# Performance work log

Hardware: AMD Instinct MI355X
Metric: run time of the kernel (lower is better)

## Reference

```python
import jax, jax.numpy as jnp
import numpy as np
import math

N_HEADS = 16  # matches init_kwargs n_heads


def setup_inputs() -> dict:
    key = jax.random.key(0)
    k1, k2, k3 = jax.random.split(key, 3)
    B, S, D = 8, 1024, 1024
    x = jax.random.normal(k1, (B, S, D), dtype=jnp.float32)
    Wc = jax.random.normal(k2, (D, 3 * D), dtype=jnp.float32) * 0.02
    bc = jnp.zeros((3 * D,), dtype=jnp.float32)
    Wo = jax.random.normal(k3, (D, D), dtype=jnp.float32) * 0.02
    bo = jnp.zeros((D,), dtype=jnp.float32)
    return {"x": x, "Wc": Wc, "bc": bc, "Wo": Wo, "bo": bo}


def reference(x, Wc, bc, Wo, bo):
    B, S, D = x.shape
    H = N_HEADS
    hd = D // H
    qkv = x @ Wc + bc                         # [B,S,3D]
    q, k, v = jnp.split(qkv, 3, axis=2)
    q = q.reshape(B, S, H, hd)
    k = k.reshape(B, S, H, hd)
    v = v.reshape(B, S, H, hd)
    # NOTE: source scales by sqrt(d_size), not sqrt(head_dim)
    scores = jnp.einsum("bqhd,bkhd->bhqk", q, k) / math.sqrt(D)
    # source mask: triu(ones) kept, zeros (k < q) filled with float32 min
    # i.e. attend only to positions k >= q (anti-causal, faithful to source)
    keep = jnp.triu(jnp.ones((S, S), dtype=bool))  # [S,S]
    neg = jnp.finfo(jnp.float32).min
    scores = jnp.where(keep[None, None, :, :], scores, neg)
    attn = jax.nn.softmax(scores, axis=-1)    # [B,H,S,S]; dropout p=0 -> identity
    out = jnp.einsum("bhqk,bkhd->bqhd", attn, v)
    concat = out.reshape(B, S, D)
    return concat @ Wo + bo                   # final dropout p=0 -> identity
```

## Files before the change

kernel.cpp:

```cpp
#include <hip/hip_runtime.h>
#include <stdint.h>

typedef __attribute__((ext_vector_type(8))) short  bf16x8;
typedef __attribute__((ext_vector_type(4))) short  short4v;
typedef __attribute__((ext_vector_type(4))) float  f32x4;
typedef __attribute__((ext_vector_type(4))) float  float4v;

#define VMW(N) asm volatile("s_waitcnt vmcnt(" #N ")" ::: "memory")
#define BAR()  asm volatile("s_barrier" ::: "memory")

__device__ __forceinline__ short f2bf(float f) {
  union { float f; uint32_t u; } c; c.f = f;
  uint32_t u = c.u;
  uint32_t r = (u + 0x7FFFu + ((u >> 16) & 1u)) >> 16;
  return (short)(uint16_t)r;
}

__device__ __forceinline__ short f2bf_hw(float f) {
  return __builtin_bit_cast(short, (__bf16)f);
}

__device__ __forceinline__ void gload_lds16(const void* g, void* l) {
  __builtin_amdgcn_global_load_lds(
      (const __attribute__((address_space(1))) void*)g,
      (__attribute__((address_space(3))) void*)l, 16, 0, 0);
}

__global__ __launch_bounds__(256) void k_f32_to_bf16(
    const float* __restrict__ in, short* __restrict__ out, int n4) {
  int i = blockIdx.x * 256 + threadIdx.x;
  if (i >= n4) return;
  float4v v = *(const float4v*)(in + (size_t)i * 4);
  short4v o;
  o.x = f2bf(v.x); o.y = f2bf(v.y); o.z = f2bf(v.z); o.w = f2bf(v.w);
  *(short4v*)(out + (size_t)i * 4) = o;
}

__global__ __launch_bounds__(256) void k_transpose_bf16(
    const float* __restrict__ in, short* __restrict__ out, int R, int C) {
  __shared__ short tile[64][65];
  int bc = blockIdx.x * 64, br = blockIdx.y * 64;
  int tc = threadIdx.x & 63, tr = threadIdx.x >> 6;
#pragma unroll
  for (int i = 0; i < 64; i += 4)
    tile[tc][tr + i] = f2bf(in[(size_t)(br + tr + i) * C + bc + tc]);
  __syncthreads();
#pragma unroll
  for (int i = 0; i < 64; i += 4)
    out[(size_t)(bc + tr + i) * R + br + tc] = tile[tr + i][tc];
}

template <bool F32OUT>
__global__ __launch_bounds__(256) void k_gemm2(
    const short* __restrict__ A, const short* __restrict__ BT,
    const float* __restrict__ bias, void* __restrict__ Cout,
    int M, int N, int K, int nbn) {
  __shared__ short SM[2][2][2][128][32];
  const int tid = threadIdx.x;
  const int w = tid >> 6, l = tid & 63;
  const int fr = l & 15, fg = l >> 4;
  const int wm = w >> 1, wn = w & 1;

  const int q8 = gridDim.x >> 3;
  const int wg = (blockIdx.x & 7) * q8 + (blockIdx.x >> 3);
  const int bm = wg / nbn, bn = wg % nbn;
  const size_t brow = (size_t)bm << 7;
  const int bcol = bn << 7;

  const int NT = K >> 6;

  const int srow = l >> 2;
  const int soct = (l & 3) ^ ((l >> 3) & 3);
  const short* aG = A + (brow + srow) * (size_t)K + soct * 8;
  const short* bG = BT + ((size_t)(bcol + srow)) * K + soct * 8;
  const int slot8 = ((fg ^ ((fr >> 1) & 3)) << 3);

  f32x4 acc[4][4] = {};

#pragma unroll
  for (int s = 0; s < 6; ++s) {
    const int t = s >> 2, tau = s & 3, buf = t & 1, mat = tau & 1, kh = tau >> 1;
    const int kbase = t * 64 + kh * 32;
    const short* g0 = (mat ? bG : aG) + kbase;
#pragma unroll
    for (int j = 0; j < 2; ++j) {
      const int r0 = (w * 2 + j) * 16;
      gload_lds16(g0 + (size_t)r0 * K, (char*)&SM[buf][mat][kh][r0][0]);
    }
  }
  VMW(8);
  BAR();

  int sidx = 6;
  for (int t = 0; t < NT; ++t) {
    const int buf = t & 1;
#pragma unroll
    for (int p = 0; p < 2; ++p) {
      const int kh = p;
#pragma unroll
      for (int s = 0; s < 2; ++s) {
        if (sidx < NT * 4) {
          const int ts = sidx >> 2, tau = sidx & 3;
          const int sb = ts & 1, mat = tau & 1, skh = tau >> 1;
          const int kbase = ts * 64 + skh * 32;
          const short* g0 = (mat ? bG : aG) + kbase;
#pragma unroll
          for (int j = 0; j < 2; ++j) {
            const int r0 = (w * 2 + j) * 16;
            gload_lds16(g0 + (size_t)r0 * K, (char*)&SM[sb][mat][skh][r0][0]);
          }
          ++sidx;
        }
      }
      bf16x8 af[4], bf[4];
#pragma unroll
      for (int m = 0; m < 4; ++m)
        af[m] = *(const bf16x8*)&SM[buf][0][kh][wm * 64 + m * 16 + fr][slot8];
#pragma unroll
      for (int n = 0; n < 4; ++n)
        bf[n] = *(const bf16x8*)&SM[buf][1][kh][wn * 64 + n * 16 + fr][slot8];
      BAR();
      __builtin_amdgcn_s_setprio(1);
#pragma unroll
      for (int m = 0; m < 4; ++m)
#pragma unroll
        for (int n = 0; n < 4; ++n)
          acc[m][n] = __builtin_amdgcn_mfma_f32_16x16x32_bf16(
              af[m], bf[n], acc[m][n], 0, 0, 0);
      __builtin_amdgcn_s_setprio(0);
      if (!(t == NT - 1 && p == 1)) {
        if (t == NT - 1 && p == 0) { VMW(0); }
        else if (t == NT - 2 && p == 1) { VMW(4); }
        else { VMW(8); }
        BAR();
      }
    }
  }

#pragma unroll
  for (int n = 0; n < 4; ++n) {
    const int col = bcol + wn * 64 + n * 16 + fr;
    const float bv = bias[col];
#pragma unroll
    for (int i = 0; i < 4; ++i) {
      const size_t row = brow + (size_t)(wm * 64 + i * 16 + fg * 4);
#pragma unroll
      for (int r = 0; r < 4; ++r) {
        const float v = acc[i][n][r] + bv;
        if (F32OUT)
          ((float*)Cout)[(row + r) * (size_t)N + col] = v;
        else
          ((short*)Cout)[(row + r) * (size_t)N + col] = f2bf(v);
      }
    }
  }
}

__global__ __launch_bounds__(256) void k_attn(
    const short* __restrict__ qkv, short* __restrict__ outc, int Bn, int S) {
  __shared__ short Ks[128][64];
  __shared__ short Vt[64][136];

  const int tid = threadIdx.x;
  const int w = tid >> 6, l = tid & 63;
  const int fr = l & 15, fg = l >> 4;

  const int tq = blockIdx.x >> 7;
  const int bh = blockIdx.x & 127;
  const int h = bh & 15, b = bh >> 4;
  const int q0 = tq << 6;

  const size_t rowbase = (size_t)b * S;
  const int qcol = q0 + w * 16 + fr;

  bf16x8 qf[2];
  {
    const short* qp = qkv + (rowbase + qcol) * 3072 + h * 64 + fg * 8;
    qf[0] = *(const bf16x8*)qp;
    qf[1] = *(const bf16x8*)(qp + 32);
    const float C2 = 0.04508422f;
#pragma unroll
    for (int j = 0; j < 8; ++j) {
      union { float f; uint32_t u; } ca, cb;
      ca.u = ((uint32_t)(uint16_t)qf[0][j]) << 16;
      cb.u = ((uint32_t)(uint16_t)qf[1][j]) << 16;
      qf[0][j] = f2bf_hw(ca.f * C2);
      qf[1][j] = f2bf_hw(cb.f * C2);
    }
  }

  f32x4 o[4] = {};
  float lacc = 0.0f;

  const short* Kbase = qkv + rowbase * 3072 + 1024 + h * 64;
  const short* Vbase = qkv + rowbase * 3072 + 2048 + h * 64;

  const int c0 = tq >> 1;
  for (int c = c0; c < 8; ++c) {
    const int k0 = c << 7;
    {
      int r8 = l >> 3, slot = l & 7;
#pragma unroll
      for (int j = 0; j < 4; ++j) {
        int ch = w * 4 + j;
        int row = ch * 8 + r8;
        int d = (slot ^ (row & 7)) << 3;
        gload_lds16(Kbase + (size_t)(k0 + row) * 3072 + d,
                    (char*)&Ks[0][0] + ch * 1024);
      }
    }
    {
      int db = (tid >> 4) << 2;
#pragma unroll
      for (int kh = 0; kh < 2; ++kh) {
        int kb = ((tid & 15) << 2) + (kh << 6);
        const short* vp = Vbase + (size_t)(k0 + kb) * 3072 + db;
        short4v r0 = *(const short4v*)(vp);
        short4v r1 = *(const short4v*)(vp + 3072);
        short4v r2 = *(const short4v*)(vp + 2 * 3072);
        short4v r3 = *(const short4v*)(vp + 3 * 3072);
        short4v t0 = {r0.x, r1.x, r2.x, r3.x};
        short4v t1 = {r0.y, r1.y, r2.y, r3.y};
        short4v t2 = {r0.z, r1.z, r2.z, r3.z};
        short4v t3 = {r0.w, r1.w, r2.w, r3.w};
        *(short4v*)&Vt[db + 0][kb] = t0;
        *(short4v*)&Vt[db + 1][kb] = t1;
        *(short4v*)&Vt[db + 2][kb] = t2;
        *(short4v*)&Vt[db + 3][kb] = t3;
      }
    }
    __syncthreads();

    f32x4 st[8];
#pragma unroll
    for (int kb = 0; kb < 8; ++kb) {
      f32x4 z = {0.f, 0.f, 0.f, 0.f};
      int row = kb * 16 + fr;
      int sw = row & 7;
      bf16x8 kf0 = *(const bf16x8*)&Ks[row][(fg ^ sw) << 3];
      bf16x8 kf1 = *(const bf16x8*)&Ks[row][((4 + fg) ^ sw) << 3];
      z = __builtin_amdgcn_mfma_f32_16x16x32_bf16(kf0, qf[0], z, 0, 0, 0);
      z = __builtin_amdgcn_mfma_f32_16x16x32_bf16(kf1, qf[1], z, 0, 0, 0);
      st[kb] = z;
    }

    const bool masked = (c == c0);
#pragma unroll
    for (int kb = 0; kb < 8; ++kb)
#pragma unroll
      for (int r = 0; r < 4; ++r) {
        float e = exp2f(st[kb][r]);
        if (masked) {
          int kg = k0 + kb * 16 + fg * 4 + r;
          e = (kg < qcol) ? 0.0f : e;
        }
        st[kb][r] = e;
        lacc += e;
      }

#pragma unroll
    for (int kb2 = 0; kb2 < 4; ++kb2) {
      bf16x8 pa = {f2bf_hw(st[2 * kb2][0]),     f2bf_hw(st[2 * kb2][1]),
                   f2bf_hw(st[2 * kb2][2]),     f2bf_hw(st[2 * kb2][3]),
                   f2bf_hw(st[2 * kb2 + 1][0]), f2bf_hw(st[2 * kb2 + 1][1]),
                   f2bf_hw(st[2 * kb2 + 1][2]), f2bf_hw(st[2 * kb2 + 1][3])};
#pragma unroll
      for (int f = 0; f < 4; ++f) {
        short4v v0 = *(const short4v*)&Vt[f * 16 + fr][kb2 * 32 + fg * 4];
        short4v v1 = *(const short4v*)&Vt[f * 16 + fr][kb2 * 32 + 16 + fg * 4];
        bf16x8 vb = {v0.x, v0.y, v0.z, v0.w, v1.x, v1.y, v1.z, v1.w};
        o[f] = __builtin_amdgcn_mfma_f32_16x16x32_bf16(pa, vb, o[f], 0, 0, 0);
      }
    }
    __syncthreads();
  }

  lacc += __shfl_xor(lacc, 16, 64);
  lacc += __shfl_xor(lacc, 32, 64);
#pragma unroll
  for (int r = 0; r < 4; ++r) {
    float denom = __shfl(lacc, fg * 4 + r, 64);
    float inv = 1.0f / denom;
    size_t orow = rowbase + (size_t)(q0 + w * 16 + fg * 4 + r);
    short* op = outc + orow * 1024 + h * 64 + fr;
#pragma unroll
    for (int f = 0; f < 4; ++f) op[f * 16] = f2bf(o[f][r] * inv);
  }
}

extern "C" void kernel_launch(void* const* d_in, const int* in_sizes, int n_in,
                              void* d_out, int out_size, void* d_ws,
                              size_t ws_size, hipStream_t stream) {
  const float* x = (const float*)d_in[0];
  const float* Wc = (const float*)d_in[1];
  const float* bc = (const float*)d_in[2];
  const float* Wo = (const float*)d_in[3];
  const float* bo = (const float*)d_in[4];
  float* out = (float*)d_out;

  const int Bn = 8, S = 1024, D = 1024;
  const int M = Bn * S;

  char* ws = (char*)d_ws;
  short* xb  = (short*)(ws);
  short* wct = (short*)(ws + (size_t)16 * 1024 * 1024);
  short* wot = (short*)(ws + (size_t)22 * 1024 * 1024);
  short* qkv = (short*)(ws + (size_t)24 * 1024 * 1024);
  short* cat = (short*)(ws + (size_t)72 * 1024 * 1024);

  k_f32_to_bf16<<<(M * D / 4 + 255) / 256, 256, 0, stream>>>(x, xb, M * D / 4);
  {
    dim3 g(3 * D / 64, D / 64);
    k_transpose_bf16<<<g, 256, 0, stream>>>(Wc, wct, D, 3 * D);
  }
  {
    dim3 g(D / 64, D / 64);
    k_transpose_bf16<<<g, 256, 0, stream>>>(Wo, wot, D, D);
  }
  k_gemm2<false><<<(M / 128) * (3 * D / 128), 256, 0, stream>>>(
      xb, wct, bc, qkv, M, 3 * D, D, 3 * D / 128);
  k_attn<<<16 * 128, 256, 0, stream>>>(qkv, cat, Bn, S);
  k_gemm2<true><<<(M / 128) * (D / 128), 256, 0, stream>>>(
      cat, wot, bo, out, M, D, D, D / 128);
}
```

Before: 162.0 us.

## Prefetch next K/V tiles in attention loop and grid-stride the bf16 convert

The attention loop now issues the K tile for chunk c+1 (global-to-LDS) and the V register loads for c+1 during the current chunk's compute. The V transpose into LDS is deferred to the top of the next iteration, after a wait and barrier. This hides global load latency behind the QK and PV MFMA work, and the barrier placement is rearranged to keep the LDS reuse safe. It costs extra registers for the V prefetch, which may affect occupancy. Separately, the f32-to-bf16 conversion kernel becomes a grid-stride loop with a fixed 2048-block grid.

```diff
diff --git a/kernel.cpp b/kernel.cpp
--- a/kernel.cpp
+++ b/kernel.cpp
@@ -28,12 +28,13 @@
 
 __global__ __launch_bounds__(256) void k_f32_to_bf16(
     const float* __restrict__ in, short* __restrict__ out, int n4) {
-  int i = blockIdx.x * 256 + threadIdx.x;
-  if (i >= n4) return;
-  float4v v = *(const float4v*)(in + (size_t)i * 4);
-  short4v o;
-  o.x = f2bf(v.x); o.y = f2bf(v.y); o.z = f2bf(v.z); o.w = f2bf(v.w);
-  *(short4v*)(out + (size_t)i * 4) = o;
+  const int stride = gridDim.x * 256;
+  for (int i = blockIdx.x * 256 + threadIdx.x; i < n4; i += stride) {
+    float4v v = *(const float4v*)(in + (size_t)i * 4);
+    short4v o;
+    o.x = f2bf(v.x); o.y = f2bf(v.y); o.z = f2bf(v.z); o.w = f2bf(v.w);
+    *(short4v*)(out + (size_t)i * 4) = o;
+  }
 }
 
 __global__ __launch_bounds__(256) void k_transpose_bf16(
@@ -195,41 +196,55 @@
   const short* Kbase = qkv + rowbase * 3072 + 1024 + h * 64;
   const short* Vbase = qkv + rowbase * 3072 + 2048 + h * 64;
 
+  const int r8 = l >> 3, slot = l & 7;
+  const int vdb = (tid >> 4) << 2;
+
+#define STAGE_K(c)                                                             \
+  {                                                                            \
+    const int k0s = (c) << 7;                                                  \
+    _Pragma("unroll") for (int j = 0; j < 4; ++j) {                            \
+      int ch = w * 4 + j;                                                      \
+      int row = ch * 8 + r8;                                                   \
+      int d = (slot ^ (row & 7)) << 3;                                         \
+      gload_lds16(Kbase + (size_t)(k0s + row) * 3072 + d,                      \
+                  (char*)&Ks[0][0] + ch * 1024);                               \
+    }                                                                          \
+  }
+#define LOAD_V(c)                                                              \
+  {                                                                            \
+    const int k0s = (c) << 7;                                                  \
+    _Pragma("unroll") for (int kh = 0; kh < 2; ++kh) {                         \
+      int kb = ((tid & 15) << 2) + (kh << 6);                                  \
+      const short* vp = Vbase + (size_t)(k0s + kb) * 3072 + vdb;               \
+      vr[kh][0] = *(const short4v*)(vp);                                       \
+      vr[kh][1] = *(const short4v*)(vp + 3072);                                \
+      vr[kh][2] = *(const short4v*)(vp + 2 * 3072);                            \
+      vr[kh][3] = *(const short4v*)(vp + 3 * 3072);                            \
+    }                                                                          \
+  }
+
   const int c0 = tq >> 1;
+  short4v vr[2][4];
+  STAGE_K(c0);
+  LOAD_V(c0);
+
   for (int c = c0; c < 8; ++c) {
     const int k0 = c << 7;
-    {
-      int r8 = l >> 3, slot = l & 7;
-#pragma unroll
-      for (int j = 0; j < 4; ++j) {
-        int ch = w * 4 + j;
-        int row = ch * 8 + r8;
-        int d = (slot ^ (row & 7)) << 3;
-        gload_lds16(Kbase + (size_t)(k0 + row) * 3072 + d,
-                    (char*)&Ks[0][0] + ch * 1024);
-      }
-    }
-    {
-      int db = (tid >> 4) << 2;
-#pragma unroll
-      for (int kh = 0; kh < 2; ++kh) {
-        int kb = ((tid & 15) << 2) + (kh << 6);
-        const short* vp = Vbase + (size_t)(k0 + kb) * 3072 + db;
-        short4v r0 = *(const short4v*)(vp);
-        short4v r1 = *(const short4v*)(vp + 3072);
-        short4v r2 = *(const short4v*)(vp + 2 * 3072);
-        short4v r3 = *(const short4v*)(vp + 3 * 3072);
-        short4v t0 = {r0.x, r1.x, r2.x, r3.x};
-        short4v t1 = {r0.y, r1.y, r2.y, r3.y};
-        short4v t2 = {r0.z, r1.z, r2.z, r3.z};
-        short4v t3 = {r0.w, r1.w, r2.w, r3.w};
-        *(short4v*)&Vt[db + 0][kb] = t0;
-        *(short4v*)&Vt[db + 1][kb] = t1;
-        *(short4v*)&Vt[db + 2][kb] = t2;
-        *(short4v*)&Vt[db + 3][kb] = t3;
-      }
-    }
+    VMW(0);
     __syncthreads();
+
+#pragma unroll
+    for (int kh = 0; kh < 2; ++kh) {
+      int kb = ((tid & 15) << 2) + (kh << 6);
+      short4v t0 = {vr[kh][0].x, vr[kh][1].x, vr[kh][2].x, vr[kh][3].x};
+      short4v t1 = {vr[kh][0].y, vr[kh][1].y, vr[kh][2].y, vr[kh][3].y};
+      short4v t2 = {vr[kh][0].z, vr[kh][1].z, vr[kh][2].z, vr[kh][3].z};
+      short4v t3 = {vr[kh][0].w, vr[kh][1].w, vr[kh][2].w, vr[kh][3].w};
+      *(short4v*)&Vt[vdb + 0][kb] = t0;
+      *(short4v*)&Vt[vdb + 1][kb] = t1;
+      *(short4v*)&Vt[vdb + 2][kb] = t2;
+      *(short4v*)&Vt[vdb + 3][kb] = t3;
+    }
 
     f32x4 st[8];
 #pragma unroll
@@ -244,6 +259,8 @@
       st[kb] = z;
     }
 
+    if (c + 1 < 8) LOAD_V(c + 1);
+
     const bool masked = (c == c0);
 #pragma unroll
     for (int kb = 0; kb < 8; ++kb)
@@ -258,6 +275,10 @@
         lacc += e;
       }
 
+    __syncthreads();
+
+    if (c + 1 < 8) STAGE_K(c + 1);
+
 #pragma unroll
     for (int kb2 = 0; kb2 < 4; ++kb2) {
       bf16x8 pa = {f2bf_hw(st[2 * kb2][0]),     f2bf_hw(st[2 * kb2][1]),
@@ -272,8 +293,9 @@
         o[f] = __builtin_amdgcn_mfma_f32_16x16x32_bf16(pa, vb, o[f], 0, 0, 0);
       }
     }
-    __syncthreads();
-  }
+  }
+#undef STAGE_K
+#undef LOAD_V
 
   lacc += __shfl_xor(lacc, 16, 64);
   lacc += __shfl_xor(lacc, 32, 64);
@@ -308,7 +330,7 @@
   short* qkv = (short*)(ws + (size_t)24 * 1024 * 1024);
   short* cat = (short*)(ws + (size_t)72 * 1024 * 1024);
 
-  k_f32_to_bf16<<<(M * D / 4 + 255) / 256, 256, 0, stream>>>(x, xb, M * D / 4);
+  k_f32_to_bf16<<<2048, 256, 0, stream>>>(x, xb, M * D / 4);
   {
     dim3 g(3 * D / 64, D / 64);
     k_transpose_bf16<<<g, 256, 0, stream>>>(Wc, wct, D, 3 * D);
```

Measured after the change: 162.7 us. Within noise of the previous version (+0.4%).
